# Kernel tuning notes

Measured on AMD Instinct MI355X. Metric: run time of the kernel, lower is better.

Reference implementation:

```python
import jax, jax.numpy as jnp
import numpy as np

PH, PW, SR = 7, 7, 2          # pooled_height, pooled_width, sampling_ratio
SCALE = 0.0625                # spatial_scale (stride 16)


def setup_inputs() -> dict:
    key = jax.random.key(0)
    k1, k2, k3, k4, k5, k6 = jax.random.split(key, 6)
    B, C, H, W = 2, 256, 100, 152
    R = 1024
    features = jax.random.normal(k1, (B, C, H, W), dtype=jnp.float32)
    img_w, img_h = W / SCALE, H / SCALE  # image-space extent
    x1 = jax.random.uniform(k2, (R,)) * (img_w * 0.7)
    y1 = jax.random.uniform(k3, (R,)) * (img_h * 0.7)
    x2 = x1 + 8.0 + jax.random.uniform(k4, (R,)) * (img_w * 0.3)
    y2 = y1 + 8.0 + jax.random.uniform(k5, (R,)) * (img_h * 0.3)
    b = jax.random.randint(k6, (R,), 0, B).astype(jnp.float32)
    rois = jnp.stack([b, x1, y1, x2, y2], axis=1)
    return {"features": features, "rois": rois}


def _roi_align(features, rois):
    B, C, H, W = features.shape
    R = rois.shape[0]
    b_idx = rois[:, 0].astype(jnp.int32)
    roi_sw = rois[:, 1] * SCALE
    roi_sh = rois[:, 2] * SCALE
    roi_ew = rois[:, 3] * SCALE
    roi_eh = rois[:, 4] * SCALE
    roi_w = jnp.maximum(roi_ew - roi_sw, 1.0)
    roi_h = jnp.maximum(roi_eh - roi_sh, 1.0)
    bin_h = roi_h / PH  # [R]
    bin_w = roi_w / PW

    # sample coordinates: Sy = PH*SR rows, Sx = PW*SR cols per ROI
    sy = jnp.arange(PH * SR)
    sx = jnp.arange(PW * SR)
    # y = start + ph*bin + (i+0.5)*bin/SR, with sy = ph*SR + i
    y = roi_sh[:, None] + ((sy // SR) + ((sy % SR) + 0.5) / SR) * bin_h[:, None]  # [R, Sy]
    x = roi_sw[:, None] + ((sx // SR) + ((sx % SR) + 0.5) / SR) * bin_w[:, None]  # [R, Sx]

    Sy, Sx = PH * SR, PW * SR
    S = Sy * Sx
    Y = jnp.broadcast_to(y[:, :, None], (R, Sy, Sx)).reshape(R, S)
    X = jnp.broadcast_to(x[:, None, :], (R, Sy, Sx)).reshape(R, S)

    valid = (Y >= -1.0) & (Y <= H) & (X >= -1.0) & (X <= W)
    Yc = jnp.clip(Y, 0.0, H - 1)
    Xc = jnp.clip(X, 0.0, W - 1)
    y_lo = jnp.floor(Yc).astype(jnp.int32)
    x_lo = jnp.floor(Xc).astype(jnp.int32)
    y_hi = jnp.minimum(y_lo + 1, H - 1)
    x_hi = jnp.minimum(x_lo + 1, W - 1)
    ly = Yc - y_lo.astype(Yc.dtype)
    lx = Xc - x_lo.astype(Xc.dtype)
    hy, hx = 1.0 - ly, 1.0 - lx

    # gather: [C, B*H*W] table, joint (batch, spatial) index
    feats2 = features.transpose(1, 0, 2, 3).reshape(C, B * H * W)
    base = b_idx[:, None] * (H * W)

    def gather(yi, xi):
        return jnp.take(feats2, base + yi * W + xi, axis=1)  # [C, R, S]

    w11 = (hy * hx)[None]
    w12 = (hy * lx)[None]
    w21 = (ly * hx)[None]
    w22 = (ly * lx)[None]
    vals = (w11 * gather(y_lo, x_lo) + w12 * gather(y_lo, x_hi)
            + w21 * gather(y_hi, x_lo) + w22 * gather(y_hi, x_hi))
    vals = jnp.where(valid[None], vals, 0.0)  # [C, R, S]

    vals = vals.reshape(C, R, PH, SR, PW, SR)
    out = vals.mean(axis=(3, 5))            # average over sub-samples
    return out.transpose(1, 0, 2, 3)        # [R, C, PH, PW]


def reference(features, rois):
    return _roi_align(features, rois)
```

## Files before the change

kernel.cpp:

```cpp
#include <hip/hip_runtime.h>
#include <cstdint>
#include <cstddef>

#define RB  2
#define RC  256
#define RH  100
#define RW  152
#define RHW (RH * RW)
#define HWQ (RHW / 4)
#define RPH 7
#define RPW 7
#define RNB (RPH * RPW)
#define HTILES ((HWQ + 31) / 32)
constexpr float kScale = 0.0625f;

__device__ __forceinline__ uint32_t f2bf(float f) {
  const uint32_t u = __float_as_uint(f);
  return (u + 0x7fffu + ((u >> 16) & 1u)) >> 16;
}
#define BFLO(p) __uint_as_float((p) << 16)
#define BFHI(p) __uint_as_float((p) & 0xffff0000u)

__global__ __launch_bounds__(256) void transpose_nchw_nhwc_bf16(
    const float* __restrict__ in, uint32_t* __restrict__ out) {
  __shared__ float lds[128 * 33];
  int bid = blockIdx.x;
  const int b  = bid / (8 * HTILES);
  bid -= b * (8 * HTILES);
  const int c0 = (bid / HTILES) * 32;
  const int ht = bid - (bid / HTILES) * HTILES;
  const int t  = threadIdx.x;

  const float4* in4  = (const float4*)(in + (size_t)b * RC * RHW);
  uint32_t*     outb = out + (size_t)b * RHW * 128;

  {
    const int tx = t & 31;
    const int ty = t >> 5;
    const int qt = ht * 32 + tx;
    if (qt < HWQ) {
#pragma unroll
      for (int j = 0; j < 4; ++j) {
        const int cl = ty + 8 * j;
        const float4 v = in4[(size_t)(c0 + cl) * HWQ + qt];
        const int hwl = tx * 4;
        lds[(hwl + 0) * 33 + cl] = v.x;
        lds[(hwl + 1) * 33 + cl] = v.y;
        lds[(hwl + 2) * 33 + cl] = v.z;
        lds[(hwl + 3) * 33 + cl] = v.w;
      }
    }
  }
  __syncthreads();
  {
    const int cq = t & 7;
    const int hr = t >> 3;
#pragma unroll
    for (int j = 0; j < 4; ++j) {
      const int hwl = hr + 32 * j;
      const int hw  = ht * 128 + hwl;
      if (hw < RHW) {
        const float o0 = lds[hwl * 33 + 4 * cq + 0];
        const float o1 = lds[hwl * 33 + 4 * cq + 1];
        const float o2 = lds[hwl * 33 + 4 * cq + 2];
        const float o3 = lds[hwl * 33 + 4 * cq + 3];
        uint2 pk;
        pk.x = f2bf(o0) | (f2bf(o1) << 16);
        pk.y = f2bf(o2) | (f2bf(o3) << 16);
        ((uint2*)outb)[(size_t)hw * 64 + (c0 >> 2) + cq] = pk;
      }
    }
  }
}

__global__ __launch_bounds__(256, 8) void roi_align_gather(
    const uint32_t* __restrict__ feat,
    const float* __restrict__ rois,
    float* __restrict__ out) {
  __shared__ float4   twgt[RNB * 4];
  __shared__ int4     toff[RNB * 4];
  __shared__ uint32_t stage[64 * RNB];

  const int r    = blockIdx.x >> 1;
  const int half = blockIdx.x & 1;
  const int t    = threadIdx.x;
  const int cg   = t & 63;
  const int wg   = t >> 6;

  const float* roi = rois + (size_t)r * 5;
  int b = (int)roi[0];
  b = (b < 0) ? 0 : (b >= RB ? RB - 1 : b);
  const float sw    = roi[1] * kScale;
  const float sh    = roi[2] * kScale;
  const float ew    = roi[3] * kScale;
  const float eh    = roi[4] * kScale;
  const float bin_w = fmaxf(ew - sw, 1.0f) * (1.0f / 7.0f);
  const float bin_h = fmaxf(eh - sh, 1.0f) * (1.0f / 7.0f);

  if (t < RNB * 4) {
    const int bi = t >> 2;
    const int s  = t & 3;
    const int ph = bi / RPW;
    const int pw = bi - ph * RPW;
    const int iy = s >> 1;
    const int ix = s & 1;
    const float y  = sh + ((float)ph + (iy ? 0.75f : 0.25f)) * bin_h;
    const float x  = sw + ((float)pw + (ix ? 0.75f : 0.25f)) * bin_w;
    const float vm = ((y >= -1.0f && y <= (float)RH) &&
                      (x >= -1.0f && x <= (float)RW)) ? 1.0f : 0.0f;
    const float yc = fminf(fmaxf(y, 0.0f), (float)(RH - 1));
    const float xc = fminf(fmaxf(x, 0.0f), (float)(RW - 1));
    const int y0 = (int)yc;
    const int x0 = (int)xc;
    const int y1 = (y0 + 1 < RH) ? y0 + 1 : RH - 1;
    const int x1 = (x0 + 1 < RW) ? x0 + 1 : RW - 1;
    const float ly = yc - (float)y0;
    const float lx = xc - (float)x0;
    const float hy = 1.0f - ly;
    const float hx = 1.0f - lx;
    twgt[t] = make_float4(hy * hx * vm, hy * lx * vm, ly * hx * vm, ly * lx * vm);
    toff[t] = make_int4((y0 * RW + x0) * 128, (y0 * RW + x1) * 128,
                        (y1 * RW + x0) * 128, (y1 * RW + x1) * 128);
  }
  __syncthreads();

  const uint32_t* fb = feat + (size_t)b * RHW * 128;
  const int ln = half * 64 + cg;

#pragma unroll 1
  for (int bi = wg; bi < RNB; bi += 4) {
    const int4 o0 = toff[bi * 4 + 0];
    const int4 o1 = toff[bi * 4 + 1];
    const int4 o2 = toff[bi * 4 + 2];
    const int4 o3 = toff[bi * 4 + 3];
    const uint32_t p00 = fb[o0.x + ln], p01 = fb[o0.y + ln],
                   p02 = fb[o0.z + ln], p03 = fb[o0.w + ln];
    const uint32_t p10 = fb[o1.x + ln], p11 = fb[o1.y + ln],
                   p12 = fb[o1.z + ln], p13 = fb[o1.w + ln];
    const uint32_t p20 = fb[o2.x + ln], p21 = fb[o2.y + ln],
                   p22 = fb[o2.z + ln], p23 = fb[o2.w + ln];
    const uint32_t p30 = fb[o3.x + ln], p31 = fb[o3.y + ln],
                   p32 = fb[o3.z + ln], p33 = fb[o3.w + ln];
    const float4 w0 = twgt[bi * 4 + 0];
    const float4 w1 = twgt[bi * 4 + 1];
    const float4 w2 = twgt[bi * 4 + 2];
    const float4 w3 = twgt[bi * 4 + 3];

    float ax, ay;
    ax  = w0.x * BFLO(p00) + w0.y * BFLO(p01) + w0.z * BFLO(p02) + w0.w * BFLO(p03);
    ay  = w0.x * BFHI(p00) + w0.y * BFHI(p01) + w0.z * BFHI(p02) + w0.w * BFHI(p03);
    ax += w1.x * BFLO(p10) + w1.y * BFLO(p11) + w1.z * BFLO(p12) + w1.w * BFLO(p13);
    ay += w1.x * BFHI(p10) + w1.y * BFHI(p11) + w1.z * BFHI(p12) + w1.w * BFHI(p13);
    ax += w2.x * BFLO(p20) + w2.y * BFLO(p21) + w2.z * BFLO(p22) + w2.w * BFLO(p23);
    ay += w2.x * BFHI(p20) + w2.y * BFHI(p21) + w2.z * BFHI(p22) + w2.w * BFHI(p23);
    ax += w3.x * BFLO(p30) + w3.y * BFLO(p31) + w3.z * BFLO(p32) + w3.w * BFLO(p33);
    ay += w3.x * BFHI(p30) + w3.y * BFHI(p31) + w3.z * BFHI(p32) + w3.w * BFHI(p33);

    stage[cg * RNB + bi] = f2bf(ax * 0.25f) | (f2bf(ay * 0.25f) << 16);
  }
  __syncthreads();

  float* outr = out + (size_t)r * (RC * RNB) + half * (128 * RNB);
#pragma unroll
  for (int it = 0; it < 24; ++it) {
    const int o  = it * 256 + t;
    const int cl = o / RNB;
    const int bi = o - cl * RNB;
    const uint32_t d = stage[(cl >> 1) * RNB + bi];
    outr[o] = (cl & 1) ? BFHI(d) : BFLO(d);
  }
  if (t < 128) {
    const int o  = 24 * 256 + t;
    const int cl = o / RNB;
    const int bi = o - cl * RNB;
    const uint32_t d = stage[(cl >> 1) * RNB + bi];
    outr[o] = (cl & 1) ? BFHI(d) : BFLO(d);
  }
}

__global__ __launch_bounds__(256) void roi_align_nchw(
    const float* __restrict__ feat,
    const float* __restrict__ rois,
    float* __restrict__ out) {
  const int r = blockIdx.x;
  const int c = threadIdx.x;

  const float* roi = rois + (size_t)r * 5;
  int b = (int)roi[0];
  b = (b < 0) ? 0 : (b >= RB ? RB - 1 : b);
  const float sw    = roi[1] * kScale;
  const float sh    = roi[2] * kScale;
  const float ew    = roi[3] * kScale;
  const float eh    = roi[4] * kScale;
  const float bin_w = fmaxf(ew - sw, 1.0f) / 7.0f;
  const float bin_h = fmaxf(eh - sh, 1.0f) / 7.0f;

  const float* fb = feat + ((size_t)b * RC + c) * RHW;

  for (int bi = 0; bi < RNB; ++bi) {
    const int ph = bi / RPW;
    const int pw = bi - ph * RPW;
    float acc = 0.f;
#pragma unroll
    for (int s = 0; s < 4; ++s) {
      const int iy = s >> 1;
      const int ix = s & 1;
      const float y = sh + ((float)ph + (iy ? 0.75f : 0.25f)) * bin_h;
      const float x = sw + ((float)pw + (ix ? 0.75f : 0.25f)) * bin_w;
      if (y < -1.0f || y > (float)RH || x < -1.0f || x > (float)RW) continue;

      const float yc = fminf(fmaxf(y, 0.0f), (float)(RH - 1));
      const float xc = fminf(fmaxf(x, 0.0f), (float)(RW - 1));
      const int y0 = (int)yc;
      const int x0 = (int)xc;
      const int y1 = (y0 + 1 < RH) ? y0 + 1 : RH - 1;
      const int x1 = (x0 + 1 < RW) ? x0 + 1 : RW - 1;
      const float ly = yc - (float)y0;
      const float lx = xc - (float)x0;
      const float hy = 1.0f - ly;
      const float hx = 1.0f - lx;

      acc += (hy * hx) * fb[y0 * RW + x0] + (hy * lx) * fb[y0 * RW + x1] +
             (ly * hx) * fb[y1 * RW + x0] + (ly * lx) * fb[y1 * RW + x1];
    }
    out[((size_t)r * RC + c) * RNB + bi] = acc * 0.25f;
  }
}

extern "C" void kernel_launch(void* const* d_in, const int* in_sizes, int n_in,
                              void* d_out, int out_size, void* d_ws, size_t ws_size,
                              hipStream_t stream) {
  const float* feat = (const float*)d_in[0];
  const float* rois = (const float*)d_in[1];
  float* out = (float*)d_out;
  const int R = in_sizes[1] / 5;

  const size_t need = (size_t)RB * RHW * RC * sizeof(uint16_t);
  const bool aligned16 =
      (((uintptr_t)d_ws | (uintptr_t)d_in[0] | (uintptr_t)d_out) & 15) == 0;

  if (ws_size >= need && aligned16 && d_ws != nullptr) {
    uint32_t* nhwc = (uint32_t*)d_ws;
    transpose_nchw_nhwc_bf16<<<RB * 8 * HTILES, 256, 0, stream>>>(feat, nhwc);
    roi_align_gather<<<R * 2, 256, 0, stream>>>(nhwc, rois, out);
  } else {
    roi_align_nchw<<<R, 256, 0, stream>>>(feat, rois, out);
  }
}
```

Baseline: 113.6 us.

## Rewrite transpose without LDS and widen gather loads with prefetch and lane split

The NCHW-to-NHWC bf16 transpose drops its shared-memory tile. Each thread now loads two adjacent channels and writes packed channel pairs straight to global memory. The gather kernel reads 8-byte uint2 words (4 channels) instead of 4-byte words. Each wave splits a bin's 16 bilinear taps across two half-waves, combines the partial sums with a cross-lane shuffle, and prefetches the next bin's features one iteration ahead. The 0.25 averaging factor is folded into the weights, and occupancy is lowered from 8 to 6 blocks per SM. This should cut load instruction count and hide gather latency, at the cost of more registers and 4-byte scattered stores in the transpose.

```diff
diff --git a/kernel.cpp b/kernel.cpp
--- a/kernel.cpp
+++ b/kernel.cpp
@@ -11,7 +11,6 @@
 #define RPH 7
 #define RPW 7
 #define RNB (RPH * RPW)
-#define HTILES ((HWQ + 31) / 32)
 constexpr float kScale = 0.0625f;
 
 __device__ __forceinline__ uint32_t f2bf(float f) {
@@ -23,68 +22,53 @@
 
 __global__ __launch_bounds__(256) void transpose_nchw_nhwc_bf16(
     const float* __restrict__ in, uint32_t* __restrict__ out) {
-  __shared__ float lds[128 * 33];
   int bid = blockIdx.x;
-  const int b  = bid / (8 * HTILES);
-  bid -= b * (8 * HTILES);
-  const int c0 = (bid / HTILES) * 32;
-  const int ht = bid - (bid / HTILES) * HTILES;
-  const int t  = threadIdx.x;
+  const int b    = bid / (2 * 950);
+  bid -= b * (2 * 950);
+  const int cgrp = bid / 950;
+  const int ht   = bid - cgrp * 950;
+  const int t    = threadIdx.x;
+  const int w    = t >> 6;
+  const int l    = t & 63;
+  const int cp   = l & 15;
+  const int q    = l >> 4;
 
   const float4* in4  = (const float4*)(in + (size_t)b * RC * RHW);
-  uint32_t*     outb = out + (size_t)b * RHW * 128;
-
-  {
-    const int tx = t & 31;
-    const int ty = t >> 5;
-    const int qt = ht * 32 + tx;
-    if (qt < HWQ) {
-#pragma unroll
-      for (int j = 0; j < 4; ++j) {
-        const int cl = ty + 8 * j;
-        const float4 v = in4[(size_t)(c0 + cl) * HWQ + qt];
-        const int hwl = tx * 4;
-        lds[(hwl + 0) * 33 + cl] = v.x;
-        lds[(hwl + 1) * 33 + cl] = v.y;
-        lds[(hwl + 2) * 33 + cl] = v.z;
-        lds[(hwl + 3) * 33 + cl] = v.w;
-      }
-    }
-  }
-  __syncthreads();
-  {
-    const int cq = t & 7;
-    const int hr = t >> 3;
-#pragma unroll
-    for (int j = 0; j < 4; ++j) {
-      const int hwl = hr + 32 * j;
-      const int hw  = ht * 128 + hwl;
-      if (hw < RHW) {
-        const float o0 = lds[hwl * 33 + 4 * cq + 0];
-        const float o1 = lds[hwl * 33 + 4 * cq + 1];
-        const float o2 = lds[hwl * 33 + 4 * cq + 2];
-        const float o3 = lds[hwl * 33 + 4 * cq + 3];
-        uint2 pk;
-        pk.x = f2bf(o0) | (f2bf(o1) << 16);
-        pk.y = f2bf(o2) | (f2bf(o3) << 16);
-        ((uint2*)outb)[(size_t)hw * 64 + (c0 >> 2) + cq] = pk;
-      }
-    }
-  }
-}
-
-__global__ __launch_bounds__(256, 8) void roi_align_gather(
+  uint32_t*     outu = out + (size_t)b * RHW * 128;
+
+  const int ch0 = cgrp * 128 + w * 32 + 2 * cp;
+  const int qt  = ht * 4 + q;
+
+  const float4 vA = in4[(size_t)ch0 * HWQ + qt];
+  const float4 vB = in4[(size_t)(ch0 + 1) * HWQ + qt];
+
+  uint32_t d0 = f2bf(vA.x) | (f2bf(vB.x) << 16);
+  uint32_t d1 = f2bf(vA.y) | (f2bf(vB.y) << 16);
+  uint32_t d2 = f2bf(vA.z) | (f2bf(vB.z) << 16);
+  uint32_t d3 = f2bf(vA.w) | (f2bf(vB.w) << 16);
+
+  const int cpg = ch0 >> 1;
+  uint32_t* o = outu + (size_t)(qt * 4) * 128 + cpg;
+  o[0 * 128] = d0;
+  o[1 * 128] = d1;
+  o[2 * 128] = d2;
+  o[3 * 128] = d3;
+}
+
+__global__ __launch_bounds__(256, 6) void roi_align_gather(
     const uint32_t* __restrict__ feat,
     const float* __restrict__ rois,
     float* __restrict__ out) {
-  __shared__ float4   twgt[RNB * 4];
-  __shared__ int4     toff[RNB * 4];
+  __shared__ float4   twgt_pe[RNB * 4];
+  __shared__ int4     toff_pe[RNB * 4];
   __shared__ uint32_t stage[64 * RNB];
 
   const int r    = blockIdx.x >> 1;
   const int half = blockIdx.x & 1;
   const int t    = threadIdx.x;
   const int cg   = t & 63;
+  const int dwp  = cg & 31;
+  const int cpar = cg >> 5;
   const int wg   = t >> 6;
 
   const float* roi = rois + (size_t)r * 5;
@@ -107,7 +91,7 @@
     const float y  = sh + ((float)ph + (iy ? 0.75f : 0.25f)) * bin_h;
     const float x  = sw + ((float)pw + (ix ? 0.75f : 0.25f)) * bin_w;
     const float vm = ((y >= -1.0f && y <= (float)RH) &&
-                      (x >= -1.0f && x <= (float)RW)) ? 1.0f : 0.0f;
+                      (x >= -1.0f && x <= (float)RW)) ? 0.25f : 0.0f;
     const float yc = fminf(fmaxf(y, 0.0f), (float)(RH - 1));
     const float xc = fminf(fmaxf(x, 0.0f), (float)(RW - 1));
     const int y0 = (int)yc;
@@ -118,45 +102,72 @@
     const float lx = xc - (float)x0;
     const float hy = 1.0f - ly;
     const float hx = 1.0f - lx;
-    twgt[t] = make_float4(hy * hx * vm, hy * lx * vm, ly * hx * vm, ly * lx * vm);
-    toff[t] = make_int4((y0 * RW + x0) * 128, (y0 * RW + x1) * 128,
-                        (y1 * RW + x0) * 128, (y1 * RW + x1) * 128);
+    const float wc[4] = {hy * hx * vm, hy * lx * vm, ly * hx * vm, ly * lx * vm};
+    const int   oc[4] = {(y0 * RW + x0) * 64, (y0 * RW + x1) * 64,
+                         (y1 * RW + x0) * 64, (y1 * RW + x1) * 64};
+    float* tw = (float*)twgt_pe;
+    int*   to = (int*)toff_pe;
+#pragma unroll
+    for (int c = 0; c < 4; ++c) {
+      const int kl = s * 4 + c;
+      const int p  = kl & 1;
+      const int j  = kl >> 1;
+      tw[(bi * 2 + p) * 8 + j] = wc[c];
+      to[(bi * 2 + p) * 8 + j] = oc[c];
+    }
   }
   __syncthreads();
 
-  const uint32_t* fb = feat + (size_t)b * RHW * 128;
-  const int ln = half * 64 + cg;
-
-#pragma unroll 1
-  for (int bi = wg; bi < RNB; bi += 4) {
-    const int4 o0 = toff[bi * 4 + 0];
-    const int4 o1 = toff[bi * 4 + 1];
-    const int4 o2 = toff[bi * 4 + 2];
-    const int4 o3 = toff[bi * 4 + 3];
-    const uint32_t p00 = fb[o0.x + ln], p01 = fb[o0.y + ln],
-                   p02 = fb[o0.z + ln], p03 = fb[o0.w + ln];
-    const uint32_t p10 = fb[o1.x + ln], p11 = fb[o1.y + ln],
-                   p12 = fb[o1.z + ln], p13 = fb[o1.w + ln];
-    const uint32_t p20 = fb[o2.x + ln], p21 = fb[o2.y + ln],
-                   p22 = fb[o2.z + ln], p23 = fb[o2.w + ln];
-    const uint32_t p30 = fb[o3.x + ln], p31 = fb[o3.y + ln],
-                   p32 = fb[o3.z + ln], p33 = fb[o3.w + ln];
-    const float4 w0 = twgt[bi * 4 + 0];
-    const float4 w1 = twgt[bi * 4 + 1];
-    const float4 w2 = twgt[bi * 4 + 2];
-    const float4 w3 = twgt[bi * 4 + 3];
-
-    float ax, ay;
-    ax  = w0.x * BFLO(p00) + w0.y * BFLO(p01) + w0.z * BFLO(p02) + w0.w * BFLO(p03);
-    ay  = w0.x * BFHI(p00) + w0.y * BFHI(p01) + w0.z * BFHI(p02) + w0.w * BFHI(p03);
-    ax += w1.x * BFLO(p10) + w1.y * BFLO(p11) + w1.z * BFLO(p12) + w1.w * BFLO(p13);
-    ay += w1.x * BFHI(p10) + w1.y * BFHI(p11) + w1.z * BFHI(p12) + w1.w * BFHI(p13);
-    ax += w2.x * BFLO(p20) + w2.y * BFLO(p21) + w2.z * BFLO(p22) + w2.w * BFLO(p23);
-    ay += w2.x * BFHI(p20) + w2.y * BFHI(p21) + w2.z * BFHI(p22) + w2.w * BFHI(p23);
-    ax += w3.x * BFLO(p30) + w3.y * BFLO(p31) + w3.z * BFLO(p32) + w3.w * BFLO(p33);
-    ay += w3.x * BFHI(p30) + w3.y * BFHI(p31) + w3.z * BFHI(p32) + w3.w * BFHI(p33);
-
-    stage[cg * RNB + bi] = f2bf(ax * 0.25f) | (f2bf(ay * 0.25f) << 16);
+  const uint2* fb2 = (const uint2*)feat + (size_t)b * RHW * 64;
+  const int ln = half * 32 + dwp;
+
+  int bi = wg;
+  int4 o0 = toff_pe[(bi * 2 + cpar) * 2 + 0];
+  int4 o1 = toff_pe[(bi * 2 + cpar) * 2 + 1];
+  uint2 p0 = fb2[o0.x + ln], p1 = fb2[o0.y + ln];
+  uint2 p2 = fb2[o0.z + ln], p3 = fb2[o0.w + ln];
+  uint2 p4 = fb2[o1.x + ln], p5 = fb2[o1.y + ln];
+  uint2 p6 = fb2[o1.z + ln], p7 = fb2[o1.w + ln];
+
+  while (true) {
+    const int nbi = bi + 4;
+    const bool more = nbi < RNB;
+    uint2 q0, q1, q2, q3, q4, q5, q6, q7;
+    if (more) {
+      const int4 no0 = toff_pe[(nbi * 2 + cpar) * 2 + 0];
+      const int4 no1 = toff_pe[(nbi * 2 + cpar) * 2 + 1];
+      q0 = fb2[no0.x + ln]; q1 = fb2[no0.y + ln];
+      q2 = fb2[no0.z + ln]; q3 = fb2[no0.w + ln];
+      q4 = fb2[no1.x + ln]; q5 = fb2[no1.y + ln];
+      q6 = fb2[no1.z + ln]; q7 = fb2[no1.w + ln];
+    }
+    const float4 w0 = twgt_pe[(bi * 2 + cpar) * 2 + 0];
+    const float4 w1 = twgt_pe[(bi * 2 + cpar) * 2 + 1];
+
+    float a0, a1, a2, a3;
+    a0  = w0.x * BFLO(p0.x) + w0.y * BFLO(p1.x) + w0.z * BFLO(p2.x) + w0.w * BFLO(p3.x);
+    a0 += w1.x * BFLO(p4.x) + w1.y * BFLO(p5.x) + w1.z * BFLO(p6.x) + w1.w * BFLO(p7.x);
+    a1  = w0.x * BFHI(p0.x) + w0.y * BFHI(p1.x) + w0.z * BFHI(p2.x) + w0.w * BFHI(p3.x);
+    a1 += w1.x * BFHI(p4.x) + w1.y * BFHI(p5.x) + w1.z * BFHI(p6.x) + w1.w * BFHI(p7.x);
+    a2  = w0.x * BFLO(p0.y) + w0.y * BFLO(p1.y) + w0.z * BFLO(p2.y) + w0.w * BFLO(p3.y);
+    a2 += w1.x * BFLO(p4.y) + w1.y * BFLO(p5.y) + w1.z * BFLO(p6.y) + w1.w * BFLO(p7.y);
+    a3  = w0.x * BFHI(p0.y) + w0.y * BFHI(p1.y) + w0.z * BFHI(p2.y) + w0.w * BFHI(p3.y);
+    a3 += w1.x * BFHI(p4.y) + w1.y * BFHI(p5.y) + w1.z * BFHI(p6.y) + w1.w * BFHI(p7.y);
+
+    a0 += __shfl_xor(a0, 32, 64);
+    a1 += __shfl_xor(a1, 32, 64);
+    a2 += __shfl_xor(a2, 32, 64);
+    a3 += __shfl_xor(a3, 32, 64);
+
+    if (cpar == 0) {
+      stage[(2 * dwp) * RNB + bi]     = f2bf(a0) | (f2bf(a1) << 16);
+      stage[(2 * dwp + 1) * RNB + bi] = f2bf(a2) | (f2bf(a3) << 16);
+    }
+
+    if (!more) break;
+    bi = nbi;
+    p0 = q0; p1 = q1; p2 = q2; p3 = q3;
+    p4 = q4; p5 = q5; p6 = q6; p7 = q7;
   }
   __syncthreads();
 
@@ -165,15 +176,15 @@
   for (int it = 0; it < 24; ++it) {
     const int o  = it * 256 + t;
     const int cl = o / RNB;
-    const int bi = o - cl * RNB;
-    const uint32_t d = stage[(cl >> 1) * RNB + bi];
+    const int bn = o - cl * RNB;
+    const uint32_t d = stage[(cl >> 1) * RNB + bn];
     outr[o] = (cl & 1) ? BFHI(d) : BFLO(d);
   }
   if (t < 128) {
     const int o  = 24 * 256 + t;
     const int cl = o / RNB;
-    const int bi = o - cl * RNB;
-    const uint32_t d = stage[(cl >> 1) * RNB + bi];
+    const int bn = o - cl * RNB;
+    const uint32_t d = stage[(cl >> 1) * RNB + bn];
     outr[o] = (cl & 1) ? BFHI(d) : BFLO(d);
   }
 }
@@ -241,7 +252,7 @@
 
   if (ws_size >= need && aligned16 && d_ws != nullptr) {
     uint32_t* nhwc = (uint32_t*)d_ws;
-    transpose_nchw_nhwc_bf16<<<RB * 8 * HTILES, 256, 0, stream>>>(feat, nhwc);
+    transpose_nchw_nhwc_bf16<<<RB * 2 * 950, 256, 0, stream>>>(feat, nhwc);
     roi_align_gather<<<R * 2, 256, 0, stream>>>(nhwc, rois, out);
   } else {
     roi_align_nchw<<<R, 256, 0, stream>>>(feat, rois, out);
```

Measured after the change: 119.1 us. +4.9%, slower.
